# Performance work log

Measured on AMD Instinct MI355X. Metric: run time of the kernel, lower is better.

The kernel has to match this reference:

```python
import jax, jax.numpy as jnp
import numpy as np

N_UP = 16

def setup_inputs() -> dict:
    key = jax.random.key(0)
    ks = jax.random.split(key, 12)
    B, n_el, n_ion = 1024, 32, 8
    d_one, d_two, d_ion, d_elion, emb = 256, 32, 64, 32, 64
    s = 0.1
    return {
        'h_one': jax.random.normal(ks[0], (B, n_el, d_one), jnp.float32),
        'h_ion': jax.random.normal(ks[1], (B, n_ion, d_ion), jnp.float32),
        'h_el_el': jax.random.normal(ks[2], (B, n_el, n_el, d_two), jnp.float32),
        'h_el_ion': jax.random.normal(ks[3], (B, n_el, n_ion, d_elion), jnp.float32),
        'W_hmap': jax.random.normal(ks[4], (d_one, emb), jnp.float32) * s,
        'b_hmap': jax.random.normal(ks[5], (emb,), jnp.float32) * s,
        'W_wsame': jax.random.normal(ks[6], (d_two, emb), jnp.float32) * s,
        'b_wsame': jax.random.normal(ks[7], (emb,), jnp.float32) * s,
        'W_wdiff': jax.random.normal(ks[8], (d_two, emb), jnp.float32) * s,
        'b_wdiff': jax.random.normal(ks[9], (emb,), jnp.float32) * s,
        'W_ion': jax.random.normal(ks[10], (d_ion, d_elion), jnp.float32) * s,
        'b_ion': jax.random.normal(ks[11], (d_elion,), jnp.float32) * s,
    }

def reference(h_one, h_ion, h_el_el, h_el_ion, W_hmap, b_hmap,
              W_wsame, b_wsame, W_wdiff, b_wdiff, W_ion, b_ion):
    n_up = N_UP
    n_el = h_one.shape[-2]
    # --- symmetric one-electron averages (use_average_h_one, same_diff=False) ---
    avg_up = jnp.mean(h_one[..., :n_up, :], axis=-2, keepdims=True)   # [B,1,d_one]
    avg_dn = jnp.mean(h_one[..., n_up:, :], axis=-2, keepdims=True)
    tile_up = jnp.broadcast_to(avg_up, h_one.shape)
    tile_dn = jnp.broadcast_to(avg_dn, h_one.shape)
    # --- two-electron averages (use_average_h_two) over second electron index ---
    f_pairs_up = jnp.mean(h_el_el[..., :n_up, :], axis=-2)  # [B,n_el,d_two]
    f_pairs_dn = jnp.mean(h_el_el[..., n_up:, :], axis=-2)
    # --- SchNet-style convolutional features ---
    # w mapping: single-layer MLP (Linear+tanh); applying per spin block is
    # identical math to the reshape/concat/MLP in the original (row-wise op).
    uu = h_el_el[..., :n_up, :n_up, :]
    ud = h_el_el[..., :n_up, n_up:, :]
    du = h_el_el[..., n_up:, :n_up, :]
    dd = h_el_el[..., n_up:, n_up:, :]
    w_uu = jnp.tanh(uu @ W_wsame + b_wsame)
    w_dd = jnp.tanh(dd @ W_wsame + b_wsame)
    w_ud = jnp.tanh(ud @ W_wdiff + b_wdiff)
    w_du = jnp.tanh(du @ W_wdiff + b_wdiff)
    h_mapped = jnp.tanh(h_one @ W_hmap + b_hmap)           # [B,n_el,emb]
    h_u = h_mapped[..., None, :n_up, :]                    # [B,1,n_up,emb]
    h_d = h_mapped[..., None, n_up:, :]
    mult_uu = w_uu * h_u
    mult_ud = w_ud * h_d
    mult_du = w_du * h_u
    mult_dd = w_dd * h_d
    emb_up = jnp.mean(mult_uu, axis=-2) + jnp.mean(mult_ud, axis=-2)
    emb_dn = jnp.mean(mult_du, axis=-2) + jnp.mean(mult_dd, axis=-2)
    el_el = jnp.concatenate([emb_up, emb_dn], axis=-2)     # [B,n_el,emb]
    h_ion_mapped = jnp.tanh(h_ion @ W_ion + b_ion)         # [B,n_ion,d_elion]
    el_ion = jnp.mean(h_el_ion * h_ion_mapped[..., None, :, :], axis=-2)
    el_el_mult = jnp.concatenate([
        jnp.concatenate([mult_uu, mult_ud], axis=-2),
        jnp.concatenate([mult_du, mult_dd], axis=-2)], axis=-3)  # [B,n_el,n_el,emb]
    feats = jnp.concatenate(
        [h_one, tile_up, tile_dn, f_pairs_up, f_pairs_dn, el_el, el_ion], axis=-1)
    return feats, el_el_mult
```

## Files before the change

### kernel.cpp

```cpp
#include <hip/hip_runtime.h>
#include <hip/hip_bf16.h>


#define FEATS_ELEMS 30408704ull
#define FD 928

typedef __attribute__((ext_vector_type(8))) short bfrag8;
typedef __attribute__((ext_vector_type(4))) float vf4;
typedef __attribute__((ext_vector_type(4))) unsigned short us4;

static __device__ __forceinline__ unsigned short f2bf(float f) {
    unsigned int u = __builtin_bit_cast(unsigned int, f);
    unsigned int r = (u + 0x7FFFu + ((u >> 16) & 1u)) >> 16;
    return (unsigned short)r;
}
static __device__ __forceinline__ float bf2f(unsigned short u) {
    unsigned int v = ((unsigned int)u) << 16;
    return __builtin_bit_cast(float, v);
}
static __device__ __forceinline__ float fast_tanh(float x) {
    float e = __expf(2.f * x);
    return 1.f - 2.f * __builtin_amdgcn_rcpf(e + 1.f);
}

__global__ __launch_bounds__(256) void sf_k1(
    const float* __restrict__ h_one,
    const float* __restrict__ h_ion,
    const float* __restrict__ W_hmap,
    const float* __restrict__ b_hmap,
    const float* __restrict__ W_ion,
    const float* __restrict__ b_ion,
    float* __restrict__ feats,
    float* __restrict__ hmap_ws,
    float* __restrict__ hion_ws)
{
    __shared__ unsigned short s_hbf[32 * 264];
    const int b = blockIdx.x;
    const int t = threadIdx.x;

    const float* hb = h_one + (size_t)b * 8192;
    float su = 0.f, sd = 0.f;
    #pragma unroll
    for (int i = 0; i < 32; ++i) {
        float v = hb[i * 256 + t];
        s_hbf[i * 264 + t] = f2bf(v);
        if (i < 16) su += v; else sd += v;
        feats[(size_t)(b * 32 + i) * FD + t] = v;
    }
    su *= (1.f / 16.f);
    sd *= (1.f / 16.f);
    #pragma unroll
    for (int i = 0; i < 32; ++i) {
        size_t row = (size_t)(b * 32 + i) * FD;
        feats[row + 256 + t] = su;
        feats[row + 512 + t] = sd;
    }

    {
        const int ai = t >> 5, kk = t & 31;
        float d = b_ion[kk];
        const float* hi = h_ion + (size_t)b * 512 + ai * 64;
        #pragma unroll 8
        for (int k2 = 0; k2 < 64; ++k2) d += hi[k2] * W_ion[k2 * 32 + kk];
        hion_ws[(size_t)b * 256 + ai * 32 + kk] = fast_tanh(d);
    }
    __syncthreads();

    const int lane  = t & 63;
    const int nt    = t >> 6;
    const int col15 = lane & 15;
    const int quad  = lane >> 4;
    const int col   = nt * 16 + col15;

    float bh = b_hmap[col];
    vf4 acc0 = {bh, bh, bh, bh};
    vf4 acc1 = acc0;
    #pragma unroll
    for (int ks = 0; ks < 8; ++ks) {
        bfrag8 bf;
        #pragma unroll
        for (int ii = 0; ii < 8; ++ii) {
            int k = ks * 32 + quad * 8 + ii;
            bf[ii] = (short)f2bf(W_hmap[k * 64 + col]);
        }
        const bfrag8 a0 = *(const bfrag8*)(s_hbf + col15 * 264 + ks * 32 + quad * 8);
        const bfrag8 a1 = *(const bfrag8*)(s_hbf + (16 + col15) * 264 + ks * 32 + quad * 8);
        acc0 = __builtin_amdgcn_mfma_f32_16x16x32_bf16(a0, bf, acc0, 0, 0, 0);
        acc1 = __builtin_amdgcn_mfma_f32_16x16x32_bf16(a1, bf, acc1, 0, 0, 0);
    }
    #pragma unroll
    for (int r = 0; r < 4; ++r) {
        int j0 = quad * 4 + r;
        hmap_ws[(size_t)(b * 32 + j0) * 64 + col]      = fast_tanh(acc0[r]);
        hmap_ws[(size_t)(b * 32 + 16 + j0) * 64 + col] = fast_tanh(acc1[r]);
    }
}

__global__ __launch_bounds__(256) void sf_k2(
    const float* __restrict__ h_el_el,
    const float* __restrict__ h_el_ion,
    const float* __restrict__ W_wsame,
    const float* __restrict__ b_wsame,
    const float* __restrict__ W_wdiff,
    const float* __restrict__ b_wdiff,
    const float* __restrict__ hmap_ws,
    const float* __restrict__ hion_ws,
    float* __restrict__ feats,
    float* __restrict__ mult_out)
{
    __shared__ unsigned short s_hee[4 * 32 * 40];
    __shared__ float s_hmap[32 * 68];
    const int b  = blockIdx.x >> 3;
    const int i0 = (blockIdx.x & 7) * 4;
    const int t  = threadIdx.x;

    {
        const float* src = h_el_el + (size_t)(b * 32 + i0) * 1024;
        #pragma unroll
        for (int r = 0; r < 4; ++r) {
            int c = r * 256 + t;
            vf4 v = ((const vf4*)src)[c];
            int g = 4 * c;
            int row = g >> 5;
            int k = g & 31;
            us4 wq = { f2bf(v[0]), f2bf(v[1]), f2bf(v[2]), f2bf(v[3]) };
            *(us4*)(s_hee + row * 40 + k) = wq;
        }
        const float* hm = hmap_ws + (size_t)b * 2048;
        #pragma unroll
        for (int r = 0; r < 2; ++r) {
            int c = r * 256 + t;
            vf4 v = ((const vf4*)hm)[c];
            int g = 4 * c;
            int row = g >> 6;
            int cc = g & 63;
            *(vf4*)(s_hmap + row * 68 + cc) = v;
        }
    }

    const int lane  = t & 63;
    const int wv    = t >> 6;
    const int i     = i0 + wv;
    const int col15 = lane & 15;
    const int quad  = lane >> 4;

    bfrag8 bs_fr[4], bd_fr[4];
    #pragma unroll
    for (int nt = 0; nt < 4; ++nt) {
        #pragma unroll
        for (int ii = 0; ii < 8; ++ii) {
            int k = quad * 8 + ii;
            int n = nt * 16 + col15;
            bs_fr[nt][ii] = (short)f2bf(W_wsame[k * 64 + n]);
            bd_fr[nt][ii] = (short)f2bf(W_wdiff[k * 64 + n]);
        }
    }
    __syncthreads();

    const unsigned short* hrow = s_hee + wv * 1280;
    const bfrag8 a_up = *(const bfrag8*)(hrow + col15 * 40 + quad * 8);
    const bfrag8 a_dn = *(const bfrag8*)(hrow + (16 + col15) * 40 + quad * 8);

    const bool iup = (i < 16);
    float* mrow = mult_out + (size_t)(b * 32 + i) * 2048;
    const size_t frow = (size_t)(b * 32 + i) * FD;

    #pragma unroll
    for (int nt = 0; nt < 4; ++nt) {
        const int col = nt * 16 + col15;
        float vbs = b_wsame[col], vbd = b_wdiff[col];
        float bu = iup ? vbs : vbd;
        float bd = iup ? vbd : vbs;
        bfrag8 fu = iup ? bs_fr[nt] : bd_fr[nt];
        bfrag8 fd = iup ? bd_fr[nt] : bs_fr[nt];
        vf4 cu = {bu, bu, bu, bu};
        vf4 cd = {bd, bd, bd, bd};
        cu = __builtin_amdgcn_mfma_f32_16x16x32_bf16(a_up, fu, cu, 0, 0, 0);
        cd = __builtin_amdgcn_mfma_f32_16x16x32_bf16(a_dn, fd, cd, 0, 0, 0);
        float s = 0.f;
        #pragma unroll
        for (int r = 0; r < 4; ++r) {
            int ju = quad * 4 + r;
            float mu = fast_tanh(cu[r]) * s_hmap[ju * 68 + col];
            mrow[ju * 64 + col] = mu;
            int jd = 16 + ju;
            float md = fast_tanh(cd[r]) * s_hmap[jd * 68 + col];
            mrow[jd * 64 + col] = md;
            s += mu + md;
        }
        s += __shfl_xor(s, 16, 64);
        s += __shfl_xor(s, 32, 64);
        if (quad == 0) feats[frow + 832 + col] = s * (1.f / 16.f);
    }

    {
        const int k = lane & 31;
        const int jb = (lane < 32) ? 0 : 16;
        float s = 0.f;
        #pragma unroll
        for (int j = 0; j < 16; ++j) s += bf2f(hrow[(jb + j) * 40 + k]);
        feats[frow + 768 + lane] = s * (1.f / 16.f);
    }

    if (lane < 32) {
        const float* hei = h_el_ion + (size_t)(b * 32 + i) * 256;
        const float* him = hion_ws + (size_t)b * 256;
        float s = 0.f;
        #pragma unroll
        for (int a = 0; a < 8; ++a) s += hei[a * 32 + lane] * him[a * 32 + lane];
        feats[frow + 896 + lane] = s * (1.f / 8.f);
    }
}

extern "C" void kernel_launch(void* const* d_in, const int* in_sizes, int n_in,
                              void* d_out, int out_size, void* d_ws, size_t ws_size,
                              hipStream_t stream) {
    const float* h_one    = (const float*)d_in[0];
    const float* h_ion    = (const float*)d_in[1];
    const float* h_el_el  = (const float*)d_in[2];
    const float* h_el_ion = (const float*)d_in[3];
    const float* W_hmap   = (const float*)d_in[4];
    const float* b_hmap   = (const float*)d_in[5];
    const float* W_wsame  = (const float*)d_in[6];
    const float* b_wsame  = (const float*)d_in[7];
    const float* W_wdiff  = (const float*)d_in[8];
    const float* b_wdiff  = (const float*)d_in[9];
    const float* W_ion    = (const float*)d_in[10];
    const float* b_ion    = (const float*)d_in[11];

    float* feats    = (float*)d_out;
    float* mult_out = feats + FEATS_ELEMS;

    float* hmap_ws = (float*)d_ws;
    float* hion_ws = hmap_ws + 1024 * 32 * 64;

    sf_k1<<<1024, 256, 0, stream>>>(h_one, h_ion, W_hmap, b_hmap, W_ion, b_ion,
                                    feats, hmap_ws, hion_ws);
    sf_k2<<<1024 * 8, 256, 0, stream>>>(h_el_el, h_el_ion, W_wsame, b_wsame,
                                        W_wdiff, b_wdiff, hmap_ws, hion_ws,
                                        feats, mult_out);
}
```

Baseline: 566.9 us.

## Pre-transpose bf16 weights, vectorize h_one pass, load h_el_el directly into registers

Measured after the change: 571.0 us. No clear change (+0.7%).

```diff
diff --git a/kernel.cpp b/kernel.cpp
--- a/kernel.cpp
+++ b/kernel.cpp
@@ -23,10 +23,31 @@
     return 1.f - 2.f * __builtin_amdgcn_rcpf(e + 1.f);
 }
 
+__global__ __launch_bounds__(256) void sf_prep(
+    const float* __restrict__ W_hmap,
+    const float* __restrict__ W_wsame,
+    const float* __restrict__ W_wdiff,
+    unsigned short* __restrict__ WhT,
+    unsigned short* __restrict__ WsT,
+    unsigned short* __restrict__ WdT)
+{
+    int e = blockIdx.x * 256 + threadIdx.x;
+    if (e < 16384) {
+        int n = e >> 8, k = e & 255;
+        WhT[e] = f2bf(W_hmap[k * 64 + n]);
+    } else if (e < 18432) {
+        int q = e - 16384;
+        WsT[q] = f2bf(W_wsame[(q & 31) * 64 + (q >> 5)]);
+    } else if (e < 20480) {
+        int q = e - 18432;
+        WdT[q] = f2bf(W_wdiff[(q & 31) * 64 + (q >> 5)]);
+    }
+}
+
 __global__ __launch_bounds__(256) void sf_k1(
     const float* __restrict__ h_one,
     const float* __restrict__ h_ion,
-    const float* __restrict__ W_hmap,
+    const unsigned short* __restrict__ WhT,
     const float* __restrict__ b_hmap,
     const float* __restrict__ W_ion,
     const float* __restrict__ b_ion,
@@ -35,26 +56,24 @@
     float* __restrict__ hion_ws)
 {
     __shared__ unsigned short s_hbf[32 * 264];
+    __shared__ vf4 s_part[4][64];
     const int b = blockIdx.x;
     const int t = threadIdx.x;
+    const int cg = t & 63;
+    const int rg = t >> 6;
 
     const float* hb = h_one + (size_t)b * 8192;
-    float su = 0.f, sd = 0.f;
-    #pragma unroll
-    for (int i = 0; i < 32; ++i) {
-        float v = hb[i * 256 + t];
-        s_hbf[i * 264 + t] = f2bf(v);
-        if (i < 16) su += v; else sd += v;
-        feats[(size_t)(b * 32 + i) * FD + t] = v;
-    }
-    su *= (1.f / 16.f);
-    sd *= (1.f / 16.f);
-    #pragma unroll
-    for (int i = 0; i < 32; ++i) {
-        size_t row = (size_t)(b * 32 + i) * FD;
-        feats[row + 256 + t] = su;
-        feats[row + 512 + t] = sd;
-    }
+    vf4 acc = {0.f, 0.f, 0.f, 0.f};
+    #pragma unroll
+    for (int r8 = 0; r8 < 8; ++r8) {
+        const int row = rg * 8 + r8;
+        vf4 v = ((const vf4*)hb)[row * 64 + cg];
+        acc = acc + v;
+        us4 w = { f2bf(v[0]), f2bf(v[1]), f2bf(v[2]), f2bf(v[3]) };
+        *(us4*)(s_hbf + row * 264 + cg * 4) = w;
+        *(vf4*)(feats + (size_t)(b * 32 + row) * FD + cg * 4) = v;
+    }
+    s_part[rg][cg] = acc;
 
     {
         const int ai = t >> 5, kk = t & 31;
@@ -66,6 +85,18 @@
     }
     __syncthreads();
 
+    {
+        vf4 su = (s_part[0][cg] + s_part[1][cg]) * (1.f / 16.f);
+        vf4 sd = (s_part[2][cg] + s_part[3][cg]) * (1.f / 16.f);
+        #pragma unroll
+        for (int r8 = 0; r8 < 8; ++r8) {
+            const int row = rg * 8 + r8;
+            size_t base = (size_t)(b * 32 + row) * FD;
+            *(vf4*)(feats + base + 256 + cg * 4) = su;
+            *(vf4*)(feats + base + 512 + cg * 4) = sd;
+        }
+    }
+
     const int lane  = t & 63;
     const int nt    = t >> 6;
     const int col15 = lane & 15;
@@ -77,12 +108,7 @@
     vf4 acc1 = acc0;
     #pragma unroll
     for (int ks = 0; ks < 8; ++ks) {
-        bfrag8 bf;
-        #pragma unroll
-        for (int ii = 0; ii < 8; ++ii) {
-            int k = ks * 32 + quad * 8 + ii;
-            bf[ii] = (short)f2bf(W_hmap[k * 64 + col]);
-        }
+        const bfrag8 bf = *(const bfrag8*)(WhT + col * 256 + ks * 32 + quad * 8);
         const bfrag8 a0 = *(const bfrag8*)(s_hbf + col15 * 264 + ks * 32 + quad * 8);
         const bfrag8 a1 = *(const bfrag8*)(s_hbf + (16 + col15) * 264 + ks * 32 + quad * 8);
         acc0 = __builtin_amdgcn_mfma_f32_16x16x32_bf16(a0, bf, acc0, 0, 0, 0);
@@ -99,67 +125,60 @@
 __global__ __launch_bounds__(256) void sf_k2(
     const float* __restrict__ h_el_el,
     const float* __restrict__ h_el_ion,
-    const float* __restrict__ W_wsame,
+    const unsigned short* __restrict__ WsT,
+    const unsigned short* __restrict__ WdT,
     const float* __restrict__ b_wsame,
-    const float* __restrict__ W_wdiff,
     const float* __restrict__ b_wdiff,
     const float* __restrict__ hmap_ws,
     const float* __restrict__ hion_ws,
     float* __restrict__ feats,
     float* __restrict__ mult_out)
 {
-    __shared__ unsigned short s_hee[4 * 32 * 40];
     __shared__ float s_hmap[32 * 68];
     const int b  = blockIdx.x >> 3;
     const int i0 = (blockIdx.x & 7) * 4;
     const int t  = threadIdx.x;
-
-    {
-        const float* src = h_el_el + (size_t)(b * 32 + i0) * 1024;
-        #pragma unroll
-        for (int r = 0; r < 4; ++r) {
-            int c = r * 256 + t;
-            vf4 v = ((const vf4*)src)[c];
-            int g = 4 * c;
-            int row = g >> 5;
-            int k = g & 31;
-            us4 wq = { f2bf(v[0]), f2bf(v[1]), f2bf(v[2]), f2bf(v[3]) };
-            *(us4*)(s_hee + row * 40 + k) = wq;
-        }
-        const float* hm = hmap_ws + (size_t)b * 2048;
-        #pragma unroll
-        for (int r = 0; r < 2; ++r) {
-            int c = r * 256 + t;
-            vf4 v = ((const vf4*)hm)[c];
-            int g = 4 * c;
-            int row = g >> 6;
-            int cc = g & 63;
-            *(vf4*)(s_hmap + row * 68 + cc) = v;
-        }
-    }
-
     const int lane  = t & 63;
     const int wv    = t >> 6;
     const int i     = i0 + wv;
     const int col15 = lane & 15;
     const int quad  = lane >> 4;
 
+    {
+        const float* hm = hmap_ws + (size_t)b * 2048;
+        #pragma unroll
+        for (int r = 0; r < 2; ++r) {
+            int c = r * 256 + t;
+            vf4 v = ((const vf4*)hm)[c];
+            int g = 4 * c;
+            *(vf4*)(s_hmap + (g >> 6) * 68 + (g & 63)) = v;
+        }
+    }
+
+    const float* hrow = h_el_el + (size_t)(b * 32 + i) * 1024;
+    const int ub = col15 * 8 + quad * 2;
+    const int db = (16 + col15) * 8 + quad * 2;
+    vf4 u0 = ((const vf4*)hrow)[ub];
+    vf4 u1 = ((const vf4*)hrow)[ub + 1];
+    vf4 d0 = ((const vf4*)hrow)[db];
+    vf4 d1 = ((const vf4*)hrow)[db + 1];
+    bfrag8 a_up, a_dn;
+    #pragma unroll
+    for (int ii = 0; ii < 4; ++ii) {
+        a_up[ii]     = (short)f2bf(u0[ii]);
+        a_up[ii + 4] = (short)f2bf(u1[ii]);
+        a_dn[ii]     = (short)f2bf(d0[ii]);
+        a_dn[ii + 4] = (short)f2bf(d1[ii]);
+    }
+
     bfrag8 bs_fr[4], bd_fr[4];
     #pragma unroll
     for (int nt = 0; nt < 4; ++nt) {
-        #pragma unroll
-        for (int ii = 0; ii < 8; ++ii) {
-            int k = quad * 8 + ii;
-            int n = nt * 16 + col15;
-            bs_fr[nt][ii] = (short)f2bf(W_wsame[k * 64 + n]);
-            bd_fr[nt][ii] = (short)f2bf(W_wdiff[k * 64 + n]);
-        }
+        const int n = nt * 16 + col15;
+        bs_fr[nt] = *(const bfrag8*)(WsT + n * 32 + quad * 8);
+        bd_fr[nt] = *(const bfrag8*)(WdT + n * 32 + quad * 8);
     }
     __syncthreads();
-
-    const unsigned short* hrow = s_hee + wv * 1280;
-    const bfrag8 a_up = *(const bfrag8*)(hrow + col15 * 40 + quad * 8);
-    const bfrag8 a_dn = *(const bfrag8*)(hrow + (16 + col15) * 40 + quad * 8);
 
     const bool iup = (i < 16);
     float* mrow = mult_out + (size_t)(b * 32 + i) * 2048;
@@ -194,12 +213,27 @@
     }
 
     {
-        const int k = lane & 31;
-        const int jb = (lane < 32) ? 0 : 16;
-        float s = 0.f;
-        #pragma unroll
-        for (int j = 0; j < 16; ++j) s += bf2f(hrow[(jb + j) * 40 + k]);
-        feats[frow + 768 + lane] = s * (1.f / 16.f);
+        float vU[8], vD[8];
+        #pragma unroll
+        for (int ii = 0; ii < 8; ++ii) {
+            vU[ii] = bf2f((unsigned short)a_up[ii]);
+            vD[ii] = bf2f((unsigned short)a_dn[ii]);
+        }
+        #pragma unroll
+        for (int m = 1; m <= 8; m <<= 1) {
+            #pragma unroll
+            for (int ii = 0; ii < 8; ++ii) {
+                vU[ii] += __shfl_xor(vU[ii], m, 64);
+                vD[ii] += __shfl_xor(vD[ii], m, 64);
+            }
+        }
+        if (col15 == 0) {
+            #pragma unroll
+            for (int ii = 0; ii < 8; ++ii) {
+                feats[frow + 768 + quad * 8 + ii] = vU[ii] * (1.f / 16.f);
+                feats[frow + 800 + quad * 8 + ii] = vD[ii] * (1.f / 16.f);
+            }
+        }
     }
 
     if (lane < 32) {
@@ -233,10 +267,14 @@
 
     float* hmap_ws = (float*)d_ws;
     float* hion_ws = hmap_ws + 1024 * 32 * 64;
-
-    sf_k1<<<1024, 256, 0, stream>>>(h_one, h_ion, W_hmap, b_hmap, W_ion, b_ion,
+    unsigned short* WhT = (unsigned short*)(hion_ws + 1024 * 8 * 32);
+    unsigned short* WsT = WhT + 16384;
+    unsigned short* WdT = WsT + 2048;
+
+    sf_prep<<<80, 256, 0, stream>>>(W_hmap, W_wsame, W_wdiff, WhT, WsT, WdT);
+    sf_k1<<<1024, 256, 0, stream>>>(h_one, h_ion, WhT, b_hmap, W_ion, b_ion,
                                     feats, hmap_ws, hion_ws);
-    sf_k2<<<1024 * 8, 256, 0, stream>>>(h_el_el, h_el_ion, W_wsame, b_wsame,
-                                        W_wdiff, b_wdiff, hmap_ws, hion_ws,
+    sf_k2<<<1024 * 8, 256, 0, stream>>>(h_el_el, h_el_ion, WsT, WdT,
+                                        b_wsame, b_wdiff, hmap_ws, hion_ws,
                                         feats, mult_out);
 }
```
